# Optimization experiments

Measured on AMD Instinct MI355X. Metric: run time of the kernel, lower is better.

Reference implementation:

```python
import jax, jax.numpy as jnp
import numpy as np

S, D, H, DK, DV = 2048, 1024, 16, 64, 64


def setup_inputs() -> dict:
    key = jax.random.key(0)
    ks = jax.random.split(key, 7)
    sc = 1.0 / np.sqrt(D)
    return {
        "encodings_for_q": jax.random.normal(ks[0], (S, D), jnp.float32),
        "encodings_for_k": jax.random.normal(ks[1], (S, D), jnp.float32),
        "encodings_for_v": jax.random.normal(ks[2], (S, D), jnp.float32),
        # per-head projection weights, stacked over heads (math-equivalent to
        # num_heads separate bias-free nn.Linear layers)
        "W_q": jax.random.normal(ks[3], (H, D, DK), jnp.float32) * sc,
        "W_k": jax.random.normal(ks[4], (H, D, DK), jnp.float32) * sc,
        "W_v": jax.random.normal(ks[5], (H, D, DV), jnp.float32) * sc,
        "W_out": jax.random.normal(ks[6], (H * DV, D), jnp.float32) * sc,
    }


def reference(encodings_for_q, encodings_for_k, encodings_for_v, W_q, W_k, W_v, W_out):
    # per-head projections: [H, S, dk/dv]
    q = jnp.einsum("sd,hdk->hsk", encodings_for_q, W_q)
    k = jnp.einsum("sd,hdk->hsk", encodings_for_k, W_k)
    v = jnp.einsum("sd,hdv->hsv", encodings_for_v, W_v)
    # scaled dot-product attention; scale = sqrt(d_k) (k.size(col_dim))
    sims = jnp.einsum("hsk,htk->hst", q, k) / jnp.sqrt(jnp.asarray(DK, q.dtype))
    attn = jax.nn.softmax(sims, axis=-1)
    ctx = jnp.einsum("hst,htv->hsv", attn, v)  # [H, S, dv]
    # concat heads along feature dim (head-major order, like torch.cat)
    cat = jnp.transpose(ctx, (1, 0, 2)).reshape(S, H * DV)
    return cat @ W_out
```

## Files before the change

kernel.cpp:

```cpp
#include <hip/hip_runtime.h>
#include <hip/hip_bf16.h>

typedef __attribute__((ext_vector_type(8))) short bf16x8;
typedef __attribute__((ext_vector_type(4))) float f32x4;

#define S_  2048
#define D_  1024
#define H_  16
#define QK_SCALE 0.18033688011f

__device__ __forceinline__ unsigned short f2bf(float x) {
    union { float f; unsigned u; } v; v.f = x;
    unsigned r = v.u + 0x7fffu + ((v.u >> 16) & 1u);
    return (unsigned short)(r >> 16);
}

__device__ __forceinline__ float bf2f(unsigned short s) {
    union { unsigned u; float f; } v; v.u = (unsigned)s << 16; return v.f;
}

__device__ __forceinline__ unsigned short bfbits(float x) {
    union { __hip_bfloat16 h; unsigned short s; } c;
    c.h = __float2bfloat16(x);
    return c.s;
}

__device__ __forceinline__ void gload16(const unsigned short* g, unsigned short* l) {
    __builtin_amdgcn_global_load_lds((const __attribute__((address_space(1))) void*)g,
                                     (__attribute__((address_space(3))) void*)l, 16, 0, 0);
}

__device__ __forceinline__ void drain_vm() {
    asm volatile("s_waitcnt vmcnt(0)" ::: "memory");
}

__global__ __launch_bounds__(256) void prep(
    const float* __restrict__ eq, const float* __restrict__ ek, const float* __restrict__ ev,
    const float* __restrict__ wq, const float* __restrict__ wk, const float* __restrict__ wv,
    const float* __restrict__ wo,
    unsigned short* __restrict__ oeq, unsigned short* __restrict__ oek,
    unsigned short* __restrict__ oev, unsigned short* __restrict__ owq,
    unsigned short* __restrict__ owk, unsigned short* __restrict__ owv,
    unsigned short* __restrict__ owo) {
    const int bx = blockIdx.x, tid = threadIdx.x;
    if (bx < 6144) {
        const float* in = bx < 2048 ? eq : bx < 4096 ? ek : ev;
        unsigned short* out = bx < 2048 ? oeq : bx < 4096 ? oek : oev;
        int i = (bx & 2047) * 256 + tid;
        float4 v = ((const float4*)in)[i];
        ushort4 o;
        o.x = f2bf(v.x); o.y = f2bf(v.y); o.z = f2bf(v.z); o.w = f2bf(v.w);
        ((ushort4*)out)[i] = o;
        return;
    }
    __shared__ float t[32][33];
    const int tx = tid & 31, ty = tid >> 5;
    if (bx < 9216) {
        int idx = bx - 6144;
        int zh = idx >> 6, rem = idx & 63;
        int which = zh >> 4, h = zh & 15;
        const float* I = (which == 0 ? wq : which == 1 ? wk : wv) + (long)h * 65536;
        unsigned short* O = (which == 0 ? owq : which == 1 ? owk : owv) + (long)h * 65536;
        float sc = which == 0 ? QK_SCALE : 1.0f;
        int c0 = (rem >> 5) * 32, r0 = (rem & 31) * 32;
        #pragma unroll
        for (int r = 0; r < 4; ++r)
            t[ty + r * 8][tx] = I[(long)(r0 + ty + r * 8) * 64 + c0 + tx];
        __syncthreads();
        #pragma unroll
        for (int r = 0; r < 4; ++r)
            O[(long)(c0 + ty + r * 8) * 1024 + r0 + tx] = f2bf(sc * t[tx][ty + r * 8]);
    } else {
        int idx = bx - 9216;
        int c0 = (idx >> 5) * 32, r0 = (idx & 31) * 32;
        #pragma unroll
        for (int r = 0; r < 4; ++r)
            t[ty + r * 8][tx] = wo[(long)(r0 + ty + r * 8) * 1024 + c0 + tx];
        __syncthreads();
        #pragma unroll
        for (int r = 0; r < 4; ++r)
            owo[(long)(c0 + ty + r * 8) * 1024 + r0 + tx] = f2bf(t[tx][ty + r * 8]);
    }
}

template<int MODE>
__device__ __forceinline__ void gemm64x128(unsigned short (*As)[64 * 64],
                                           unsigned short (*Bs)[128 * 64],
                                           const unsigned short* __restrict__ A,
                                           const unsigned short* __restrict__ Bt,
                                           void* __restrict__ C, int m0, int n0, int ldc) {
    const int tid = threadIdx.x, wv = tid >> 6, lane = tid & 63, lg = lane >> 4, lr = lane & 15;
    f32x4 acc[4][2] = {};
    const unsigned short* Ab = A + (size_t)m0 * D_;
    const unsigned short* Bb = Bt + (size_t)n0 * D_;
    auto stage = [&](int b, int kt) {
        #pragma unroll
        for (int it = 0; it < 2; ++it) {
            int c = it * 256 + wv * 64 + lane;
            int row = c >> 3, jj = (c & 7) ^ (row & 7);
            gload16(Ab + (size_t)row * D_ + kt * 64 + jj * 8, &As[b][(it * 256 + wv * 64) * 8]);
        }
        #pragma unroll
        for (int it = 0; it < 4; ++it) {
            int c = it * 256 + wv * 64 + lane;
            int row = c >> 3, jj = (c & 7) ^ (row & 7);
            gload16(Bb + (size_t)row * D_ + kt * 64 + jj * 8, &Bs[b][(it * 256 + wv * 64) * 8]);
        }
    };
    stage(0, 0);
    drain_vm();
    __syncthreads();
    int buf = 0;
    for (int kt = 0; kt < 16; ++kt) {
        if (kt + 1 < 16) stage(buf ^ 1, kt + 1);
        #pragma unroll
        for (int kk = 0; kk < 2; ++kk) {
            bf16x8 af[4], bfr[2];
            #pragma unroll
            for (int mf = 0; mf < 4; ++mf) {
                int r = mf * 16 + lr;
                af[mf] = *(const bf16x8*)&As[buf][(r * 8 + ((kk * 4 + lg) ^ (r & 7))) * 8];
            }
            #pragma unroll
            for (int nf = 0; nf < 2; ++nf) {
                int r = wv * 32 + nf * 16 + lr;
                bfr[nf] = *(const bf16x8*)&Bs[buf][(r * 8 + ((kk * 4 + lg) ^ (r & 7))) * 8];
            }
            #pragma unroll
            for (int mf = 0; mf < 4; ++mf)
                #pragma unroll
                for (int nf = 0; nf < 2; ++nf)
                    acc[mf][nf] = __builtin_amdgcn_mfma_f32_16x16x32_bf16(af[mf], bfr[nf], acc[mf][nf], 0, 0, 0);
        }
        drain_vm();
        __syncthreads();
        buf ^= 1;
    }
    #pragma unroll
    for (int mf = 0; mf < 4; ++mf)
        #pragma unroll
        for (int nf = 0; nf < 2; ++nf) {
            if (MODE == 1) {
                int gn = n0 + wv * 32 + nf * 16 + lr;
                int pg = m0 + (mf >> 1) * 32 + lg * 8 + (mf & 1) * 4;
                ushort4 pk;
                pk.x = f2bf(acc[mf][nf][0]); pk.y = f2bf(acc[mf][nf][1]);
                pk.z = f2bf(acc[mf][nf][2]); pk.w = f2bf(acc[mf][nf][3]);
                *(ushort4*)&((unsigned short*)C)[(size_t)gn * ldc + pg] = pk;
            } else {
                #pragma unroll
                for (int j = 0; j < 4; ++j) {
                    int gm = m0 + mf * 16 + lg * 4 + j;
                    int gn = n0 + wv * 32 + nf * 16 + lr;
                    ((unsigned short*)C)[(size_t)gm * ldc + gn] = f2bf(acc[mf][nf][j]);
                }
            }
        }
}

__global__ __launch_bounds__(256, 3) void proj_kernel(
    const unsigned short* __restrict__ Eq, const unsigned short* __restrict__ Ek,
    const unsigned short* __restrict__ Ev, const unsigned short* __restrict__ Wqt,
    const unsigned short* __restrict__ Wkt, const unsigned short* __restrict__ Wvt,
    unsigned short* __restrict__ Qb, unsigned short* __restrict__ Kb,
    unsigned short* __restrict__ Vtb) {
    __shared__ alignas(16) unsigned short As[2][64 * 64];
    __shared__ alignas(16) unsigned short Bs[2][128 * 64];
    int m0 = blockIdx.x * 64, n0 = blockIdx.y * 128;
    if (blockIdx.z == 0)      gemm64x128<0>(As, Bs, Eq, Wqt, Qb, m0, n0, 1024);
    else if (blockIdx.z == 1) gemm64x128<0>(As, Bs, Ek, Wkt, Kb, m0, n0, 1024);
    else                      gemm64x128<1>(As, Bs, Ev, Wvt, Vtb, m0, n0, S_);
}

__global__ __launch_bounds__(256, 2) void out_gemm(const unsigned short* __restrict__ Cat,
                                                   const unsigned short* __restrict__ Wot,
                                                   float* __restrict__ Out) {
    __shared__ alignas(16) unsigned short As[2][64 * 64];
    __shared__ alignas(16) unsigned short Bs[2][64 * 64];
    const int tid = threadIdx.x, wv = tid >> 6, lane = tid & 63, lg = lane >> 4, lr = lane & 15;
    int m0 = blockIdx.x * 64, n0 = blockIdx.y * 64;
    f32x4 acc[4] = {};
    const unsigned short* Ab = Cat + (size_t)m0 * D_;
    const unsigned short* Bb = Wot + (size_t)n0 * D_;
    auto stage = [&](int b, int kt) {
        #pragma unroll
        for (int it = 0; it < 2; ++it) {
            int c = it * 256 + wv * 64 + lane;
            int row = c >> 3, jj = (c & 7) ^ (row & 7);
            gload16(Ab + (size_t)row * D_ + kt * 64 + jj * 8, &As[b][(it * 256 + wv * 64) * 8]);
        }
        #pragma unroll
        for (int it = 0; it < 2; ++it) {
            int c = it * 256 + wv * 64 + lane;
            int row = c >> 3, jj = (c & 7) ^ (row & 7);
            gload16(Bb + (size_t)row * D_ + kt * 64 + jj * 8, &Bs[b][(it * 256 + wv * 64) * 8]);
        }
    };
    stage(0, 0);
    drain_vm();
    __syncthreads();
    int buf = 0;
    for (int kt = 0; kt < 16; ++kt) {
        if (kt + 1 < 16) stage(buf ^ 1, kt + 1);
        #pragma unroll
        for (int kk = 0; kk < 2; ++kk) {
            int ra = wv * 16 + lr;
            bf16x8 af = *(const bf16x8*)&As[buf][(ra * 8 + ((kk * 4 + lg) ^ (ra & 7))) * 8];
            #pragma unroll
            for (int nf = 0; nf < 4; ++nf) {
                int r = nf * 16 + lr;
                bf16x8 bfr = *(const bf16x8*)&Bs[buf][(r * 8 + ((kk * 4 + lg) ^ (r & 7))) * 8];
                acc[nf] = __builtin_amdgcn_mfma_f32_16x16x32_bf16(af, bfr, acc[nf], 0, 0, 0);
            }
        }
        drain_vm();
        __syncthreads();
        buf ^= 1;
    }
    #pragma unroll
    for (int nf = 0; nf < 4; ++nf)
        #pragma unroll
        for (int j = 0; j < 4; ++j)
            Out[(size_t)(m0 + wv * 16 + lg * 4 + j) * 1024 + n0 + nf * 16 + lr] = acc[nf][j];
}

__global__ __launch_bounds__(256, 4) void attn_kernel(
    const unsigned short* __restrict__ Qb, const unsigned short* __restrict__ Kb,
    const unsigned short* __restrict__ Vtb, unsigned short* __restrict__ Opb,
    float* __restrict__ Ml) {
    __shared__ alignas(16) unsigned short Ks[2][64 * 64];
    __shared__ alignas(16) unsigned short Vs[2][64 * 64];

    const int h = blockIdx.y, s0 = blockIdx.x * 128;
    const int tid = threadIdx.x, wv = tid >> 6, lane = tid & 63, lg = lane >> 4, lr = lane & 15;

    const unsigned short* qrA = Qb + (size_t)(s0 + wv * 32 + lr) * D_ + h * 64;
    const unsigned short* qrB = qrA + 16 * D_;
    const bf16x8 qA0 = *(const bf16x8*)(qrA + lg * 8);
    const bf16x8 qA1 = *(const bf16x8*)(qrA + 32 + lg * 8);
    const bf16x8 qB0 = *(const bf16x8*)(qrB + lg * 8);
    const bf16x8 qB1 = *(const bf16x8*)(qrB + 32 + lg * 8);

    float mA = 0.f, mB = 0.f, lA = 0.f, lB = 0.f;
    f32x4 oA[4] = {}, oB[4] = {};

    const unsigned short* KhB = Kb + h * 64;
    const unsigned short* VhB = Vtb + (size_t)(h * 64) * S_;

    auto stage = [&](int b, int t) {
        #pragma unroll
        for (int it = 0; it < 2; ++it) {
            int c = it * 256 + wv * 64 + lane;
            int row = c >> 3, jj = (c & 7) ^ (row & 7);
            gload16(KhB + (size_t)(t * 64 + row) * D_ + jj * 8, &Ks[b][(it * 256 + wv * 64) * 8]);
        }
        #pragma unroll
        for (int it = 0; it < 2; ++it) {
            int c = it * 256 + wv * 64 + lane;
            int row = c >> 3, jj = (c & 7) ^ (row & 7);
            gload16(VhB + (size_t)row * S_ + t * 64 + jj * 8, &Vs[b][(it * 256 + wv * 64) * 8]);
        }
    };

    const int t0 = blockIdx.z * 8;
    stage(0, t0);
    drain_vm();
    __syncthreads();
    int buf = 0;
    for (int tt = 0; tt < 8; ++tt) {
        if (tt + 1 < 8) stage(buf ^ 1, t0 + tt + 1);
        const unsigned short* K_ = Ks[buf];
        const unsigned short* V_ = Vs[buf];

        f32x4 sa[4] = {}, sb[4] = {};
        __builtin_amdgcn_s_setprio(1);
        #pragma unroll
        for (int kk = 0; kk < 2; ++kk) {
            bf16x8 qa = kk ? qA1 : qA0;
            bf16x8 qb = kk ? qB1 : qB0;
            #pragma unroll
            for (int n = 0; n < 4; ++n) {
                int r = n * 16 + lr;
                bf16x8 kf = *(const bf16x8*)&K_[(r * 8 + ((kk * 4 + lg) ^ (r & 7))) * 8];
                sa[n] = __builtin_amdgcn_mfma_f32_16x16x32_bf16(kf, qa, sa[n], 0, 0, 0);
                sb[n] = __builtin_amdgcn_mfma_f32_16x16x32_bf16(kf, qb, sb[n], 0, 0, 0);
            }
        }
        __builtin_amdgcn_s_setprio(0);

        float mxA = sa[0][0], mxB = sb[0][0];
        #pragma unroll
        for (int n = 0; n < 4; ++n)
            #pragma unroll
            for (int j = 0; j < 4; ++j) {
                mxA = fmaxf(mxA, sa[n][j]);
                mxB = fmaxf(mxB, sb[n][j]);
            }
        if (__any((mxA > mA + 11.f) || (mxB > mB + 11.f))) {
            mxA = fmaxf(mxA, __shfl_xor(mxA, 16)); mxA = fmaxf(mxA, __shfl_xor(mxA, 32));
            mxB = fmaxf(mxB, __shfl_xor(mxB, 16)); mxB = fmaxf(mxB, __shfl_xor(mxB, 32));
            float nA = fmaxf(mA, mxA), nB = fmaxf(mB, mxB);
            float aA = exp2f(mA - nA), aB = exp2f(mB - nB);
            mA = nA; mB = nB; lA *= aA; lB *= aB;
            #pragma unroll
            for (int n = 0; n < 4; ++n) { oA[n] *= aA; oB[n] *= aB; }
        }
        float rsA = 0.f, rsB = 0.f;
        #pragma unroll
        for (int n = 0; n < 4; ++n)
            #pragma unroll
            for (int j = 0; j < 4; ++j) {
                float pa = exp2f(sa[n][j] - mA);
                float pb = exp2f(sb[n][j] - mB);
                sa[n][j] = pa; rsA += pa;
                sb[n][j] = pb; rsB += pb;
            }
        lA += rsA; lB += rsB;

        bf16x8 pA[2], pB[2];
        #pragma unroll
        for (int kk = 0; kk < 2; ++kk) {
            union { bf16x8 v; unsigned short s[8]; } ua, ub;
            #pragma unroll
            for (int i = 0; i < 4; ++i) {
                ua.s[i]     = bfbits(sa[2 * kk][i]);
                ua.s[4 + i] = bfbits(sa[2 * kk + 1][i]);
                ub.s[i]     = bfbits(sb[2 * kk][i]);
                ub.s[4 + i] = bfbits(sb[2 * kk + 1][i]);
            }
            pA[kk] = ua.v; pB[kk] = ub.v;
        }
        __builtin_amdgcn_s_setprio(1);
        #pragma unroll
        for (int n = 0; n < 4; ++n) {
            int r = n * 16 + lr;
            #pragma unroll
            for (int kk = 0; kk < 2; ++kk) {
                bf16x8 vf = *(const bf16x8*)&V_[(r * 8 + ((kk * 4 + lg) ^ (r & 7))) * 8];
                oA[n] = __builtin_amdgcn_mfma_f32_16x16x32_bf16(vf, pA[kk], oA[n], 0, 0, 0);
                oB[n] = __builtin_amdgcn_mfma_f32_16x16x32_bf16(vf, pB[kk], oB[n], 0, 0, 0);
            }
        }
        __builtin_amdgcn_s_setprio(0);
        drain_vm();
        __syncthreads();
        buf ^= 1;
    }
    lA += __shfl_xor(lA, 16); lA += __shfl_xor(lA, 32);
    lB += __shfl_xor(lB, 16); lB += __shfl_xor(lB, 32);

    const int slot = blockIdx.z * 16 + h;
    size_t qa = (size_t)s0 + wv * 32 + lr, qb = qa + 16;
    size_t baseA = ((size_t)slot * S_ + qa) * 64;
    size_t baseB = ((size_t)slot * S_ + qb) * 64;
    #pragma unroll
    for (int n = 0; n < 4; ++n) {
        ushort4 ka, kb2;
        ka.x  = f2bf(oA[n][0]); ka.y  = f2bf(oA[n][1]);
        ka.z  = f2bf(oA[n][2]); ka.w  = f2bf(oA[n][3]);
        kb2.x = f2bf(oB[n][0]); kb2.y = f2bf(oB[n][1]);
        kb2.z = f2bf(oB[n][2]); kb2.w = f2bf(oB[n][3]);
        *(ushort4*)&Opb[baseA + n * 16 + lg * 4] = ka;
        *(ushort4*)&Opb[baseB + n * 16 + lg * 4] = kb2;
    }
    if (lg == 0) {
        size_t miA = (size_t)slot * S_ + qa, miB = (size_t)slot * S_ + qb;
        Ml[miA * 2] = mA; Ml[miA * 2 + 1] = lA;
        Ml[miB * 2] = mB; Ml[miB * 2 + 1] = lB;
    }
}

__global__ __launch_bounds__(256) void combine(const unsigned short* __restrict__ Opb,
                                               const float* __restrict__ Ml,
                                               unsigned short* __restrict__ Cat) {
    int gid = blockIdx.x * 256 + threadIdx.x;
    int d4 = gid & 15, s = (gid >> 4) & 2047, h = gid >> 15;
    float m[4], l[4];
    #pragma unroll
    for (int i = 0; i < 4; ++i) {
        size_t mi = ((size_t)(i * 16 + h) * S_ + s) * 2;
        m[i] = Ml[mi]; l[i] = Ml[mi + 1];
    }
    float M = fmaxf(fmaxf(m[0], m[1]), fmaxf(m[2], m[3]));
    float w[4], denom = 0.f;
    #pragma unroll
    for (int i = 0; i < 4; ++i) { w[i] = exp2f(m[i] - M); denom += w[i] * l[i]; }
    float inv = 1.f / fmaxf(denom, 1e-30f);
    float o0 = 0.f, o1 = 0.f, o2 = 0.f, o3 = 0.f;
    #pragma unroll
    for (int i = 0; i < 4; ++i) {
        ushort4 u = *(const ushort4*)&Opb[((size_t)(i * 16 + h) * S_ + s) * 64 + d4 * 4];
        o0 += w[i] * bf2f(u.x); o1 += w[i] * bf2f(u.y);
        o2 += w[i] * bf2f(u.z); o3 += w[i] * bf2f(u.w);
    }
    ushort4 pk;
    pk.x = f2bf(o0 * inv); pk.y = f2bf(o1 * inv);
    pk.z = f2bf(o2 * inv); pk.w = f2bf(o3 * inv);
    *(ushort4*)&Cat[(size_t)s * D_ + h * 64 + d4 * 4] = pk;
}

extern "C" void kernel_launch(void* const* d_in, const int* in_sizes, int n_in,
                              void* d_out, int out_size, void* d_ws, size_t ws_size,
                              hipStream_t stream) {
    const float* enc_q = (const float*)d_in[0];
    const float* enc_k = (const float*)d_in[1];
    const float* enc_v = (const float*)d_in[2];
    const float* W_q   = (const float*)d_in[3];
    const float* W_k   = (const float*)d_in[4];
    const float* W_v   = (const float*)d_in[5];
    const float* W_out = (const float*)d_in[6];
    float* out = (float*)d_out;

    const size_t M1 = 1024 * 1024;
    unsigned short* Eqb = (unsigned short*)d_ws;
    unsigned short* Ekb = Eqb + 2 * M1;
    unsigned short* Evb = Ekb + 2 * M1;
    unsigned short* Wqt = Evb + 2 * M1;
    unsigned short* Wkt = Wqt + M1;
    unsigned short* Wvt = Wkt + M1;
    unsigned short* Wot = Wvt + M1;
    unsigned short* Qb  = Wot + M1;
    unsigned short* Kb  = Qb  + 2 * M1;
    unsigned short* Vtb = Kb  + 2 * M1;
    unsigned short* Cat = Vtb + 2 * M1;
    unsigned short* Opb = (unsigned short*)d_ws;
    float* Ml = (float*)((char*)d_ws + 17u * 1024 * 1024);

    prep<<<10240, 256, 0, stream>>>(enc_q, enc_k, enc_v, W_q, W_k, W_v, W_out,
                                    Eqb, Ekb, Evb, Wqt, Wkt, Wvt, Wot);
    proj_kernel<<<dim3(32, 8, 3), 256, 0, stream>>>(Eqb, Ekb, Evb, Wqt, Wkt, Wvt, Qb, Kb, Vtb);
    attn_kernel<<<dim3(16, 16, 4), 256, 0, stream>>>(Qb, Kb, Vtb, Opb, Ml);
    combine<<<2048, 256, 0, stream>>>(Opb, Ml, Cat);
    out_gemm<<<dim3(32, 16), 256, 0, stream>>>(Cat, Wot, out);
}
```

Before: 95.06 us.

## Software-pipeline QK^T one tile ahead with triple-buffered V in attention

The attention loop is restructured so the QK^T MFMAs for tile t+1 are issued before the softmax and PV of tile t. Score accumulators are double-buffered in registers, and V is triple-buffered in LDS with loads issued two tiles ahead. The explicit vmcnt drain at the end of each iteration is removed, the row max uses a 3-input max tree, and launch bounds drop from 4 to 3 waves per SIMD to leave room for the extra registers. The goal is to overlap matrix-core work with the exp and convert phase and with global-to-LDS loads. The costs are lower occupancy and a possible race, since nothing now explicitly waits for the async LDS loads before the barrier.

```diff
diff --git a/kernel.cpp b/kernel.cpp
--- a/kernel.cpp
+++ b/kernel.cpp
@@ -23,6 +23,10 @@
     union { __hip_bfloat16 h; unsigned short s; } c;
     c.h = __float2bfloat16(x);
     return c.s;
+}
+
+__device__ __forceinline__ float fm3(float a, float b, float c) {
+    return fmaxf(fmaxf(a, b), c);
 }
 
 __device__ __forceinline__ void gload16(const unsigned short* g, unsigned short* l) {
@@ -224,12 +228,12 @@
             Out[(size_t)(m0 + wv * 16 + lg * 4 + j) * 1024 + n0 + nf * 16 + lr] = acc[nf][j];
 }
 
-__global__ __launch_bounds__(256, 4) void attn_kernel(
+__global__ __launch_bounds__(256, 3) void attn_kernel(
     const unsigned short* __restrict__ Qb, const unsigned short* __restrict__ Kb,
     const unsigned short* __restrict__ Vtb, unsigned short* __restrict__ Opb,
     float* __restrict__ Ml) {
     __shared__ alignas(16) unsigned short Ks[2][64 * 64];
-    __shared__ alignas(16) unsigned short Vs[2][64 * 64];
+    __shared__ alignas(16) unsigned short Vs[3][64 * 64];
 
     const int h = blockIdx.y, s0 = blockIdx.x * 128;
     const int tid = threadIdx.x, wv = tid >> 6, lane = tid & 63, lg = lane >> 4, lr = lane & 15;
@@ -243,36 +247,29 @@
 
     float mA = 0.f, mB = 0.f, lA = 0.f, lB = 0.f;
     f32x4 oA[4] = {}, oB[4] = {};
+    f32x4 sa[2][4], sb[2][4];
 
     const unsigned short* KhB = Kb + h * 64;
     const unsigned short* VhB = Vtb + (size_t)(h * 64) * S_;
-
-    auto stage = [&](int b, int t) {
+    const int t0 = blockIdx.z * 8;
+
+    auto stageL = [&](int u) {
+        int t = t0 + u;
         #pragma unroll
         for (int it = 0; it < 2; ++it) {
             int c = it * 256 + wv * 64 + lane;
             int row = c >> 3, jj = (c & 7) ^ (row & 7);
-            gload16(KhB + (size_t)(t * 64 + row) * D_ + jj * 8, &Ks[b][(it * 256 + wv * 64) * 8]);
+            gload16(KhB + (size_t)(t * 64 + row) * D_ + jj * 8, &Ks[u & 1][(it * 256 + wv * 64) * 8]);
         }
         #pragma unroll
         for (int it = 0; it < 2; ++it) {
             int c = it * 256 + wv * 64 + lane;
             int row = c >> 3, jj = (c & 7) ^ (row & 7);
-            gload16(VhB + (size_t)row * S_ + t * 64 + jj * 8, &Vs[b][(it * 256 + wv * 64) * 8]);
+            gload16(VhB + (size_t)row * S_ + t * 64 + jj * 8, &Vs[u % 3][(it * 256 + wv * 64) * 8]);
         }
     };
-
-    const int t0 = blockIdx.z * 8;
-    stage(0, t0);
-    drain_vm();
-    __syncthreads();
-    int buf = 0;
-    for (int tt = 0; tt < 8; ++tt) {
-        if (tt + 1 < 8) stage(buf ^ 1, t0 + tt + 1);
-        const unsigned short* K_ = Ks[buf];
-        const unsigned short* V_ = Vs[buf];
-
-        f32x4 sa[4] = {}, sb[4] = {};
+    auto qk = [&](int u) {
+        const unsigned short* K_ = Ks[u & 1];
         __builtin_amdgcn_s_setprio(1);
         #pragma unroll
         for (int kk = 0; kk < 2; ++kk) {
@@ -282,20 +279,49 @@
             for (int n = 0; n < 4; ++n) {
                 int r = n * 16 + lr;
                 bf16x8 kf = *(const bf16x8*)&K_[(r * 8 + ((kk * 4 + lg) ^ (r & 7))) * 8];
-                sa[n] = __builtin_amdgcn_mfma_f32_16x16x32_bf16(kf, qa, sa[n], 0, 0, 0);
-                sb[n] = __builtin_amdgcn_mfma_f32_16x16x32_bf16(kf, qb, sb[n], 0, 0, 0);
+                if (kk == 0) {
+                    f32x4 z = {};
+                    sa[u & 1][n] = __builtin_amdgcn_mfma_f32_16x16x32_bf16(kf, qa, z, 0, 0, 0);
+                    sb[u & 1][n] = __builtin_amdgcn_mfma_f32_16x16x32_bf16(kf, qb, z, 0, 0, 0);
+                } else {
+                    sa[u & 1][n] = __builtin_amdgcn_mfma_f32_16x16x32_bf16(kf, qa, sa[u & 1][n], 0, 0, 0);
+                    sb[u & 1][n] = __builtin_amdgcn_mfma_f32_16x16x32_bf16(kf, qb, sb[u & 1][n], 0, 0, 0);
+                }
             }
         }
         __builtin_amdgcn_s_setprio(0);
-
-        float mxA = sa[0][0], mxB = sb[0][0];
-        #pragma unroll
-        for (int n = 0; n < 4; ++n)
-            #pragma unroll
-            for (int j = 0; j < 4; ++j) {
-                mxA = fmaxf(mxA, sa[n][j]);
-                mxB = fmaxf(mxB, sb[n][j]);
-            }
+    };
+
+    stageL(0);
+    stageL(1);
+    #pragma unroll
+    for (int tt = 0; tt < 8; ++tt) {
+        __syncthreads();
+        if (tt == 0) {
+            qk(0);
+            stageL(2);
+        } else if (tt + 2 < 8) {
+            stageL(tt + 2);
+        }
+        if (tt + 1 < 8) qk(tt + 1);
+
+        f32x4* sA = sa[tt & 1];
+        f32x4* sB = sb[tt & 1];
+        float mxA, mxB;
+        {
+            float a0 = fm3(sA[0][0], sA[0][1], sA[0][2]);
+            float a1 = fm3(sA[0][3], sA[1][0], sA[1][1]);
+            float a2 = fm3(sA[1][2], sA[1][3], sA[2][0]);
+            float a3 = fm3(sA[2][1], sA[2][2], sA[2][3]);
+            float a4 = fm3(sA[3][0], sA[3][1], sA[3][2]);
+            mxA = fm3(fm3(a0, a1, a2), fmaxf(a3, a4), sA[3][3]);
+            float b0 = fm3(sB[0][0], sB[0][1], sB[0][2]);
+            float b1 = fm3(sB[0][3], sB[1][0], sB[1][1]);
+            float b2 = fm3(sB[1][2], sB[1][3], sB[2][0]);
+            float b3 = fm3(sB[2][1], sB[2][2], sB[2][3]);
+            float b4 = fm3(sB[3][0], sB[3][1], sB[3][2]);
+            mxB = fm3(fm3(b0, b1, b2), fmaxf(b3, b4), sB[3][3]);
+        }
         if (__any((mxA > mA + 11.f) || (mxB > mB + 11.f))) {
             mxA = fmaxf(mxA, __shfl_xor(mxA, 16)); mxA = fmaxf(mxA, __shfl_xor(mxA, 32));
             mxB = fmaxf(mxB, __shfl_xor(mxB, 16)); mxB = fmaxf(mxB, __shfl_xor(mxB, 32));
@@ -310,10 +336,10 @@
         for (int n = 0; n < 4; ++n)
             #pragma unroll
             for (int j = 0; j < 4; ++j) {
-                float pa = exp2f(sa[n][j] - mA);
-                float pb = exp2f(sb[n][j] - mB);
-                sa[n][j] = pa; rsA += pa;
-                sb[n][j] = pb; rsB += pb;
+                float pa = exp2f(sA[n][j] - mA);
+                float pb = exp2f(sB[n][j] - mB);
+                sA[n][j] = pa; rsA += pa;
+                sB[n][j] = pb; rsB += pb;
             }
         lA += rsA; lB += rsB;
 
@@ -323,13 +349,14 @@
             union { bf16x8 v; unsigned short s[8]; } ua, ub;
             #pragma unroll
             for (int i = 0; i < 4; ++i) {
-                ua.s[i]     = bfbits(sa[2 * kk][i]);
-                ua.s[4 + i] = bfbits(sa[2 * kk + 1][i]);
-                ub.s[i]     = bfbits(sb[2 * kk][i]);
-                ub.s[4 + i] = bfbits(sb[2 * kk + 1][i]);
+                ua.s[i]     = bfbits(sA[2 * kk][i]);
+                ua.s[4 + i] = bfbits(sA[2 * kk + 1][i]);
+                ub.s[i]     = bfbits(sB[2 * kk][i]);
+                ub.s[4 + i] = bfbits(sB[2 * kk + 1][i]);
             }
             pA[kk] = ua.v; pB[kk] = ub.v;
         }
+        const unsigned short* V_ = Vs[tt % 3];
         __builtin_amdgcn_s_setprio(1);
         #pragma unroll
         for (int n = 0; n < 4; ++n) {
@@ -342,9 +369,6 @@
             }
         }
         __builtin_amdgcn_s_setprio(0);
-        drain_vm();
-        __syncthreads();
-        buf ^= 1;
     }
     lA += __shfl_xor(lA, 16); lA += __shfl_xor(lA, 32);
     lB += __shfl_xor(lB, 16); lB += __shfl_xor(lB, 32);
```

New measurement: 93.45 us. Within noise of the previous version (-1.7%).

## Split attention KV tiles across waves and merge partial softmax in LDS

Applied to the files above, without the earlier changes.

The attention kernel now gives each block 32 query rows. Each of the four waves processes two distinct KV tiles, reading K and V fragments directly from global memory instead of through double-buffered LDS staging with a barrier per tile. Per-wave partial outputs and max/sum statistics are merged through shared memory by wave 0, and the grid grows fourfold. This removes LDS staging and per-tile syncs and raises parallelism. In exchange, K/V reuse across query rows drops to 32 rows per block, so each tile is read from global memory or cache four times as often, and the final merge is serialized on one wave.

```diff
diff --git a/kernel.cpp b/kernel.cpp
--- a/kernel.cpp
+++ b/kernel.cpp
@@ -23,6 +23,10 @@
     union { __hip_bfloat16 h; unsigned short s; } c;
     c.h = __float2bfloat16(x);
     return c.s;
+}
+
+__device__ __forceinline__ float fm3(float a, float b, float c) {
+    return fmaxf(fmaxf(a, b), c);
 }
 
 __device__ __forceinline__ void gload16(const unsigned short* g, unsigned short* l) {
@@ -224,78 +228,65 @@
             Out[(size_t)(m0 + wv * 16 + lg * 4 + j) * 1024 + n0 + nf * 16 + lr] = acc[nf][j];
 }
 
-__global__ __launch_bounds__(256, 4) void attn_kernel(
+__global__ __launch_bounds__(256, 3) void attn_kernel(
     const unsigned short* __restrict__ Qb, const unsigned short* __restrict__ Kb,
     const unsigned short* __restrict__ Vtb, unsigned short* __restrict__ Opb,
     float* __restrict__ Ml) {
-    __shared__ alignas(16) unsigned short Ks[2][64 * 64];
-    __shared__ alignas(16) unsigned short Vs[2][64 * 64];
-
-    const int h = blockIdx.y, s0 = blockIdx.x * 128;
+    __shared__ float oSh[3][2][4][256];
+    __shared__ float mlSh[4][2][16][2];
+
+    const int h = blockIdx.y, s0 = blockIdx.x * 32;
     const int tid = threadIdx.x, wv = tid >> 6, lane = tid & 63, lg = lane >> 4, lr = lane & 15;
 
-    const unsigned short* qrA = Qb + (size_t)(s0 + wv * 32 + lr) * D_ + h * 64;
+    const unsigned short* qrA = Qb + (size_t)(s0 + lr) * D_ + h * 64;
     const unsigned short* qrB = qrA + 16 * D_;
     const bf16x8 qA0 = *(const bf16x8*)(qrA + lg * 8);
     const bf16x8 qA1 = *(const bf16x8*)(qrA + 32 + lg * 8);
     const bf16x8 qB0 = *(const bf16x8*)(qrB + lg * 8);
     const bf16x8 qB1 = *(const bf16x8*)(qrB + 32 + lg * 8);
 
+    const unsigned short* KhB = Kb + h * 64;
+    const unsigned short* VhB = Vtb + (size_t)(h * 64) * S_;
+
     float mA = 0.f, mB = 0.f, lA = 0.f, lB = 0.f;
     f32x4 oA[4] = {}, oB[4] = {};
 
-    const unsigned short* KhB = Kb + h * 64;
-    const unsigned short* VhB = Vtb + (size_t)(h * 64) * S_;
-
-    auto stage = [&](int b, int t) {
-        #pragma unroll
-        for (int it = 0; it < 2; ++it) {
-            int c = it * 256 + wv * 64 + lane;
-            int row = c >> 3, jj = (c & 7) ^ (row & 7);
-            gload16(KhB + (size_t)(t * 64 + row) * D_ + jj * 8, &Ks[b][(it * 256 + wv * 64) * 8]);
-        }
-        #pragma unroll
-        for (int it = 0; it < 2; ++it) {
-            int c = it * 256 + wv * 64 + lane;
-            int row = c >> 3, jj = (c & 7) ^ (row & 7);
-            gload16(VhB + (size_t)row * S_ + t * 64 + jj * 8, &Vs[b][(it * 256 + wv * 64) * 8]);
-        }
-    };
-
-    const int t0 = blockIdx.z * 8;
-    stage(0, t0);
-    drain_vm();
-    __syncthreads();
-    int buf = 0;
-    for (int tt = 0; tt < 8; ++tt) {
-        if (tt + 1 < 8) stage(buf ^ 1, t0 + tt + 1);
-        const unsigned short* K_ = Ks[buf];
-        const unsigned short* V_ = Vs[buf];
-
-        f32x4 sa[4] = {}, sb[4] = {};
+    #pragma unroll
+    for (int u = 0; u < 2; ++u) {
+        const int t = blockIdx.z * 8 + wv * 2 + u;
+        const unsigned short* Kt = KhB + (size_t)t * 64 * D_;
+        const unsigned short* Vt = VhB + (size_t)t * 64;
+
+        f32x4 sa[4], sb[4];
         __builtin_amdgcn_s_setprio(1);
         #pragma unroll
-        for (int kk = 0; kk < 2; ++kk) {
-            bf16x8 qa = kk ? qA1 : qA0;
-            bf16x8 qb = kk ? qB1 : qB0;
-            #pragma unroll
-            for (int n = 0; n < 4; ++n) {
-                int r = n * 16 + lr;
-                bf16x8 kf = *(const bf16x8*)&K_[(r * 8 + ((kk * 4 + lg) ^ (r & 7))) * 8];
-                sa[n] = __builtin_amdgcn_mfma_f32_16x16x32_bf16(kf, qa, sa[n], 0, 0, 0);
-                sb[n] = __builtin_amdgcn_mfma_f32_16x16x32_bf16(kf, qb, sb[n], 0, 0, 0);
-            }
+        for (int n = 0; n < 4; ++n) {
+            const unsigned short* kr = Kt + (size_t)(n * 16 + lr) * D_;
+            bf16x8 kf0 = *(const bf16x8*)(kr + lg * 8);
+            bf16x8 kf1 = *(const bf16x8*)(kr + 32 + lg * 8);
+            f32x4 z = {};
+            sa[n] = __builtin_amdgcn_mfma_f32_16x16x32_bf16(kf0, qA0, z, 0, 0, 0);
+            sa[n] = __builtin_amdgcn_mfma_f32_16x16x32_bf16(kf1, qA1, sa[n], 0, 0, 0);
+            sb[n] = __builtin_amdgcn_mfma_f32_16x16x32_bf16(kf0, qB0, z, 0, 0, 0);
+            sb[n] = __builtin_amdgcn_mfma_f32_16x16x32_bf16(kf1, qB1, sb[n], 0, 0, 0);
         }
         __builtin_amdgcn_s_setprio(0);
 
-        float mxA = sa[0][0], mxB = sb[0][0];
-        #pragma unroll
-        for (int n = 0; n < 4; ++n)
-            #pragma unroll
-            for (int j = 0; j < 4; ++j) {
-                mxA = fmaxf(mxA, sa[n][j]);
-                mxB = fmaxf(mxB, sb[n][j]);
-            }
+        float mxA, mxB;
+        {
+            float a0 = fm3(sa[0][0], sa[0][1], sa[0][2]);
+            float a1 = fm3(sa[0][3], sa[1][0], sa[1][1]);
+            float a2 = fm3(sa[1][2], sa[1][3], sa[2][0]);
+            float a3 = fm3(sa[2][1], sa[2][2], sa[2][3]);
+            float a4 = fm3(sa[3][0], sa[3][1], sa[3][2]);
+            mxA = fm3(fm3(a0, a1, a2), fmaxf(a3, a4), sa[3][3]);
+            float b0 = fm3(sb[0][0], sb[0][1], sb[0][2]);
+            float b1 = fm3(sb[0][3], sb[1][0], sb[1][1]);
+            float b2 = fm3(sb[1][2], sb[1][3], sb[2][0]);
+            float b3 = fm3(sb[2][1], sb[2][2], sb[2][3]);
+            float b4 = fm3(sb[3][0], sb[3][1], sb[3][2]);
+            mxB = fm3(fm3(b0, b1, b2), fmaxf(b3, b4), sb[3][3]);
+        }
         if (__any((mxA > mA + 11.f) || (mxB > mB + 11.f))) {
             mxA = fmaxf(mxA, __shfl_xor(mxA, 16)); mxA = fmaxf(mxA, __shfl_xor(mxA, 32));
             mxB = fmaxf(mxB, __shfl_xor(mxB, 16)); mxB = fmaxf(mxB, __shfl_xor(mxB, 32));
@@ -333,40 +324,66 @@
         __builtin_amdgcn_s_setprio(1);
         #pragma unroll
         for (int n = 0; n < 4; ++n) {
-            int r = n * 16 + lr;
+            const unsigned short* vr = Vt + (size_t)(n * 16 + lr) * S_;
             #pragma unroll
             for (int kk = 0; kk < 2; ++kk) {
-                bf16x8 vf = *(const bf16x8*)&V_[(r * 8 + ((kk * 4 + lg) ^ (r & 7))) * 8];
+                bf16x8 vf = *(const bf16x8*)(vr + (kk * 4 + lg) * 8);
                 oA[n] = __builtin_amdgcn_mfma_f32_16x16x32_bf16(vf, pA[kk], oA[n], 0, 0, 0);
                 oB[n] = __builtin_amdgcn_mfma_f32_16x16x32_bf16(vf, pB[kk], oB[n], 0, 0, 0);
             }
         }
         __builtin_amdgcn_s_setprio(0);
-        drain_vm();
-        __syncthreads();
-        buf ^= 1;
     }
     lA += __shfl_xor(lA, 16); lA += __shfl_xor(lA, 32);
     lB += __shfl_xor(lB, 16); lB += __shfl_xor(lB, 32);
 
-    const int slot = blockIdx.z * 16 + h;
-    size_t qa = (size_t)s0 + wv * 32 + lr, qb = qa + 16;
-    size_t baseA = ((size_t)slot * S_ + qa) * 64;
-    size_t baseB = ((size_t)slot * S_ + qb) * 64;
-    #pragma unroll
-    for (int n = 0; n < 4; ++n) {
-        ushort4 ka, kb2;
-        ka.x  = f2bf(oA[n][0]); ka.y  = f2bf(oA[n][1]);
-        ka.z  = f2bf(oA[n][2]); ka.w  = f2bf(oA[n][3]);
-        kb2.x = f2bf(oB[n][0]); kb2.y = f2bf(oB[n][1]);
-        kb2.z = f2bf(oB[n][2]); kb2.w = f2bf(oB[n][3]);
-        *(ushort4*)&Opb[baseA + n * 16 + lg * 4] = ka;
-        *(ushort4*)&Opb[baseB + n * 16 + lg * 4] = kb2;
+    if (wv > 0) {
+        #pragma unroll
+        for (int n = 0; n < 4; ++n)
+            #pragma unroll
+            for (int j = 0; j < 4; ++j) {
+                oSh[wv - 1][0][n][lr * 16 + lg * 4 + j] = oA[n][j];
+                oSh[wv - 1][1][n][lr * 16 + lg * 4 + j] = oB[n][j];
+            }
     }
     if (lg == 0) {
-        size_t miA = (size_t)slot * S_ + qa, miB = (size_t)slot * S_ + qb;
-        Ml[miA * 2] = mA; Ml[miA * 2 + 1] = lA;
-        Ml[miB * 2] = mB; Ml[miB * 2 + 1] = lB;
+        mlSh[wv][0][lr][0] = mA; mlSh[wv][0][lr][1] = lA;
+        mlSh[wv][1][lr][0] = mB; mlSh[wv][1][lr][1] = lB;
+    }
+    __syncthreads();
+    if (wv == 0) {
+        const int slot = blockIdx.z * 16 + h;
+        #pragma unroll
+        for (int set = 0; set < 2; ++set) {
+            float m0 = set ? mB : mA, l0 = set ? lB : lA;
+            float m1 = mlSh[1][set][lr][0], l1 = mlSh[1][set][lr][1];
+            float m2 = mlSh[2][set][lr][0], l2 = mlSh[2][set][lr][1];
+            float m3 = mlSh[3][set][lr][0], l3 = mlSh[3][set][lr][1];
+            float M = fmaxf(fmaxf(m0, m1), fmaxf(m2, m3));
+            float w0 = exp2f(m0 - M), w1 = exp2f(m1 - M);
+            float w2 = exp2f(m2 - M), w3 = exp2f(m3 - M);
+            float L = w0 * l0 + w1 * l1 + w2 * l2 + w3 * l3;
+            size_t q = (size_t)s0 + set * 16 + lr;
+            size_t base = ((size_t)slot * S_ + q) * 64;
+            const f32x4* oo = set ? oB : oA;
+            #pragma unroll
+            for (int n = 0; n < 4; ++n) {
+                ushort4 pk;
+                #pragma unroll
+                for (int j = 0; j < 4; ++j) {
+                    float v = w0 * oo[n][j]
+                            + w1 * oSh[0][set][n][lr * 16 + lg * 4 + j]
+                            + w2 * oSh[1][set][n][lr * 16 + lg * 4 + j]
+                            + w3 * oSh[2][set][n][lr * 16 + lg * 4 + j];
+                    ((unsigned short*)&pk)[j] = f2bf(v);
+                }
+                *(ushort4*)&Opb[base + n * 16 + lg * 4] = pk;
+            }
+            if (lg == 0) {
+                size_t mi = (size_t)slot * S_ + q;
+                Ml[mi * 2] = M; Ml[mi * 2 + 1] = L;
+            }
+        }
     }
 }
 
@@ -429,7 +446,7 @@
     prep<<<10240, 256, 0, stream>>>(enc_q, enc_k, enc_v, W_q, W_k, W_v, W_out,
                                     Eqb, Ekb, Evb, Wqt, Wkt, Wvt, Wot);
     proj_kernel<<<dim3(32, 8, 3), 256, 0, stream>>>(Eqb, Ekb, Evb, Wqt, Wkt, Wvt, Qb, Kb, Vtb);
-    attn_kernel<<<dim3(16, 16, 4), 256, 0, stream>>>(Qb, Kb, Vtb, Opb, Ml);
+    attn_kernel<<<dim3(64, 16, 4), 256, 0, stream>>>(Qb, Kb, Vtb, Opb, Ml);
     combine<<<2048, 256, 0, stream>>>(Opb, Ml, Cat);
     out_gemm<<<dim3(32, 16), 256, 0, stream>>>(Cat, Wot, out);
 }
```

Measured after the change: 131.0 us. 37.8% more time.
